# Kernel tuning notes

Hardware: AMD Instinct MI355X
Metric: run time of the kernel (lower is better)

The kernel has to match this reference:

```python
import jax, jax.numpy as jnp
import numpy as np

N_NODES = 50000


def _gcn_conv(h, W, b, src, dst, dinv):
    # PyG GCNConv: linear transform, then symmetric-normalized sum aggregation
    h = h @ W  # (N, d_out)
    norm = dinv[src] * dinv[dst]  # (E,)
    msg = h[src] * norm[:, None]  # (E, d_out)
    agg = jax.ops.segment_sum(msg, dst, num_segments=N_NODES)
    return agg + b


def setup_inputs() -> dict:
    key = jax.random.key(0)
    ks = jax.random.split(key, 9)
    in_dim, h1, h2, out_dim = 512, 512, 512, 256
    x = jax.random.normal(ks[0], (N_NODES, in_dim), dtype=jnp.float32)
    edge_index = jax.random.randint(ks[1], (2, 800000), 0, N_NODES, dtype=jnp.int64)

    def glorot(k, shape):
        lim = float(np.sqrt(6.0 / (shape[0] + shape[1])))
        return jax.random.uniform(k, shape, jnp.float32, -lim, lim)

    return {
        "x": x,
        "edge_index": edge_index,
        "W1": glorot(ks[2], (in_dim, h1)),
        "b1": jnp.zeros((h1,), jnp.float32),
        "W2": glorot(ks[3], (h1, h2)),
        "b2": jnp.zeros((h2,), jnp.float32),
        "Wout": glorot(ks[4], (h2, out_dim)),
        "bout": jnp.zeros((out_dim,), jnp.float32),
    }


def reference(x, edge_index, W1, b1, W2, b2, Wout, bout):
    # add self-loops (GCNConv default)
    loop = jnp.arange(N_NODES, dtype=edge_index.dtype)
    src = jnp.concatenate([edge_index[0], loop])
    dst = jnp.concatenate([edge_index[1], loop])
    # degree on A + I (target side), deg^{-1/2}
    deg = jax.ops.segment_sum(jnp.ones_like(dst, dtype=x.dtype), dst, num_segments=N_NODES)
    dinv = jnp.where(deg > 0, jax.lax.rsqrt(deg), 0.0)

    h = jax.nn.relu(_gcn_conv(x, W1, b1, src, dst, dinv))
    h = jax.nn.relu(_gcn_conv(h, W2, b2, src, dst, dinv))
    return h @ Wout + bout
```

## Files before the change

### kernel.cpp

```cpp
#include <hip/hip_runtime.h>

#define NN 50000
#define MP 50048
#define DD 512
#define EE 800000
#define NSCAN 196
#define SCB 3321
#define G1TILES 1564

typedef unsigned short u16;
typedef __attribute__((ext_vector_type(4))) float f32x4;
typedef __attribute__((ext_vector_type(8))) __bf16 bf16x8;
typedef __attribute__((ext_vector_type(8))) short s16x8;
typedef __attribute__((ext_vector_type(4))) short s16x4;

typedef __attribute__((address_space(1))) const void GVoid;
typedef __attribute__((address_space(3))) void LVoid;

__device__ __forceinline__ u16 f2bf(float f) {
  union { float f; unsigned u; } x; x.f = f;
  unsigned r = x.u + 0x7fffu + ((x.u >> 16) & 1u);
  return (u16)(r >> 16);
}
__device__ __forceinline__ float bf2f(u16 b) {
  union { unsigned u; float f; } x; x.u = ((unsigned)b) << 16;
  return x.f;
}


__global__ __launch_bounds__(256) void setup_k(int* __restrict__ cnt,
                                               const float* __restrict__ W1, u16* __restrict__ W1T,
                                               const float* __restrict__ W2, u16* __restrict__ W2T,
                                               const float* __restrict__ Wo, u16* __restrict__ WoT,
                                               int2* __restrict__ csr) {
  const int b = (int)blockIdx.x, t = threadIdx.x;
  if (b < 196) {
    int i = b * 256 + t;
    if (i < NN) cnt[i] = 1;
    if (b == 0 && t < 64) csr[EE + NN + t] = make_int2(0, 0);
    return;
  }
  const float* W; u16* WT; int ncols, idx;
  if (b < 1220)      { W = W1; WT = W1T; ncols = 512; idx = (b - 196) * 256 + t; }
  else if (b < 2244) { W = W2; WT = W2T; ncols = 512; idx = (b - 1220) * 256 + t; }
  else               { W = Wo; WT = WoT; ncols = 256; idx = (b - 2244) * 256 + t; }
  if (idx >= 512 * ncols) return;
  int n = idx >> 9, k = idx & 511;
  WT[idx] = f2bf(W[(size_t)k * ncols + n]);
}

__global__ __launch_bounds__(256) void count_k(const int* __restrict__ dst, int* __restrict__ cnt) {
  int e = blockIdx.x * 256 + threadIdx.x;
  if (e < EE) atomicAdd(&cnt[dst[e]], 1);
}


__global__ __launch_bounds__(256) void scan1_k(const int* __restrict__ cnt, int* __restrict__ bsum) {
  __shared__ int s[256];
  const int t = threadIdx.x;
  const int i = blockIdx.x * 256 + t;
  s[t] = (i < NN) ? cnt[i] : 0;
  __syncthreads();
  for (int off = 128; off > 0; off >>= 1) {
    if (t < off) s[t] += s[t + off];
    __syncthreads();
  }
  if (t == 0) bsum[blockIdx.x] = s[0];
}

__global__ __launch_bounds__(256) void scan2_k(const int* __restrict__ bsum, int* __restrict__ boff) {
  __shared__ int s[256];
  const int t = threadIdx.x;
  const int v = (t < NSCAN) ? bsum[t] : 0;
  s[t] = v;
  __syncthreads();
  for (int off = 1; off < 256; off <<= 1) {
    int a = s[t];
    int b = (t >= off) ? s[t - off] : 0;
    __syncthreads();
    s[t] = a + b;
    __syncthreads();
  }
  if (t < NSCAN) boff[t] = s[t] - v;
}

__global__ __launch_bounds__(256) void scan3_k(const int* __restrict__ cnt, const int* __restrict__ boff,
                                               int* __restrict__ rowp, int* __restrict__ cursor,
                                               float* __restrict__ dinv) {
  __shared__ int s[256];
  const int t = threadIdx.x;
  const int i = blockIdx.x * 256 + t;
  const int v = (i < NN) ? cnt[i] : 0;
  s[t] = v;
  __syncthreads();
  for (int off = 1; off < 256; off <<= 1) {
    int a = s[t];
    int b = (t >= off) ? s[t - off] : 0;
    __syncthreads();
    s[t] = a + b;
    __syncthreads();
  }
  const int excl = s[t] - v + boff[blockIdx.x];
  if (i < NN) {
    rowp[i] = excl; cursor[i] = excl;
    dinv[i] = rsqrtf((float)v);
  }
  if (i == NN - 1) rowp[NN] = excl + v;
}


__global__ __launch_bounds__(256) void gemm1_k(const float* __restrict__ X, const u16* __restrict__ BT,
                                               u16* __restrict__ C,
                                               const int* __restrict__ src, const int* __restrict__ dst,
                                               const float* __restrict__ dinv, int* __restrict__ cursor,
                                               int2* __restrict__ csr) {
  __shared__ u16 As[2][128 * 32];
  __shared__ u16 Bs[2][128 * 32];
  const int t = threadIdx.x;

  if (blockIdx.x < SCB) {
    int e = (int)blockIdx.x * 256 + t;
    if (e < EE) {
      int d = dst[e], sn = src[e];
      int pos = atomicAdd(&cursor[d], 1);
      csr[pos] = make_int2(sn, __float_as_int(dinv[sn] * dinv[d]));
    } else if (e < EE + NN) {
      int i = e - EE;
      int pos = atomicAdd(&cursor[i], 1);
      float di = dinv[i];
      csr[pos] = make_int2(i, __float_as_int(di * di));
    }
    return;
  }

  const int g = (int)blockIdx.x - SCB;
  const int xcd = g & 7;
  const int idx = g >> 3;
  const int q = G1TILES >> 3, r = G1TILES & 7;
  const int tile = (xcd < r ? xcd * (q + 1) : r * (q + 1) + (xcd - r) * q) + idx;
  const int bm = tile >> 2;
  const int bn = tile & 3;

  const int lane = t & 63;
  const int wc = (t >> 6) & 1;
  const int wr = (t >> 7) & 1;
  f32x4 acc[4][4] = {};
  const int r0 = t >> 2;
  const int kc = (t & 3) * 8;
  const int row1 = bm * 128 + 64 + r0;
  const float* Xp0 = X + (size_t)(bm * 128 + r0) * DD + kc;
  const float* Xp1 = X + (size_t)(row1 < NN ? row1 : NN - 1) * DD + kc;
  const u16* Bb = BT + (size_t)bn * 128 * DD + (size_t)r0 * DD + kc;

  f32x4 a0, a1, a2, a3;
  auto loadA = [&](int kt) {
    a0 = *(const f32x4*)(Xp0 + kt);
    a1 = *(const f32x4*)(Xp0 + kt + 4);
    a2 = *(const f32x4*)(Xp1 + kt);
    a3 = *(const f32x4*)(Xp1 + kt + 4);
  };
  auto writeA = [&](int buf) {
    bf16x8 w0, w1;
    #pragma unroll
    for (int j = 0; j < 4; ++j) {
      w0[j] = (__bf16)a0[j]; w0[4 + j] = (__bf16)a1[j];
      w1[j] = (__bf16)a2[j]; w1[4 + j] = (__bf16)a3[j];
    }
    *(bf16x8*)&As[buf][t * 8] = w0;
    *(bf16x8*)&As[buf][2048 + t * 8] = w1;
  };
  auto stageB = [&](int buf, int kt) {
    __builtin_amdgcn_global_load_lds((GVoid*)(Bb + kt),           (LVoid*)(&Bs[buf][t * 8]),        16, 0, 0);
    __builtin_amdgcn_global_load_lds((GVoid*)(Bb + 64 * DD + kt), (LVoid*)(&Bs[buf][2048 + t * 8]), 16, 0, 0);
  };

  loadA(0);
  stageB(0, 0);
  writeA(0);
  __syncthreads();

  #pragma unroll 2
  for (int step = 0; step < 16; ++step) {
    const int cur = step & 1;
    if (step < 15) { loadA((step + 1) * 32); stageB(cur ^ 1, (step + 1) * 32); }
    bf16x8 af[4], bv[4];
    #pragma unroll
    for (int m = 0; m < 4; ++m)
      af[m] = *(const bf16x8*)&As[cur][(wr * 64 + m * 16 + (lane & 15)) * 32 + (lane >> 4) * 8];
    #pragma unroll
    for (int n = 0; n < 4; ++n)
      bv[n] = *(const bf16x8*)&Bs[cur][(wc * 64 + n * 16 + (lane & 15)) * 32 + (lane >> 4) * 8];
    #pragma unroll
    for (int m = 0; m < 4; ++m) {
      #pragma unroll
      for (int n = 0; n < 4; ++n)
        acc[m][n] = __builtin_amdgcn_mfma_f32_16x16x32_bf16(af[m], bv[n], acc[m][n], 0, 0, 0);
    }
    if (step < 15) writeA(cur ^ 1);
    __syncthreads();
  }

  const int rb = bm * 128 + wr * 64 + ((lane >> 4) * 4);
  const int cb = bn * 128 + wc * 64 + (lane & 15);
  #pragma unroll
  for (int m = 0; m < 4; ++m) {
    #pragma unroll
    for (int rr = 0; rr < 4; ++rr) {
      const int row = rb + m * 16 + rr;
      if (row < NN) {
        #pragma unroll
        for (int n = 0; n < 4; ++n)
          C[(size_t)row * 512 + cb + n * 16] = f2bf(acc[m][n][rr]);
      }
    }
  }
}


template<int OUT_BF16>
__global__ __launch_bounds__(256) void gemm_k(const u16* __restrict__ A, const u16* __restrict__ BT,
                                              void* __restrict__ Cv, const float* __restrict__ bias,
                                              int M, int N) {
  const int nwg = (int)gridDim.x;
  const int id = (int)blockIdx.x;
  const int xcd = id & 7;
  const int idx = id >> 3;
  const int q = nwg >> 3, r = nwg & 7;
  const int tile = (xcd < r ? xcd * (q + 1) : r * (q + 1) + (xcd - r) * q) + idx;
  const int ntn = N >> 7;
  const int bm = tile / ntn;
  const int bn = tile % ntn;

  __shared__ u16 As[2][128 * 32];
  __shared__ u16 Bs[2][128 * 32];
  const int t = threadIdx.x;
  const int lane = t & 63;
  const int wc = (t >> 6) & 1;
  const int wr = (t >> 7) & 1;
  f32x4 acc[4][4] = {};
  const int r0 = t >> 2;
  const int kc = (t & 3) * 8;
  const u16* Ab = A + (size_t)bm * 128 * DD + (size_t)r0 * DD + kc;
  const u16* Bb = BT + (size_t)bn * 128 * DD + (size_t)r0 * DD + kc;

  auto stage = [&](int buf, int kt) {
    __builtin_amdgcn_global_load_lds((GVoid*)(Ab + kt),           (LVoid*)(&As[buf][t * 8]),        16, 0, 0);
    __builtin_amdgcn_global_load_lds((GVoid*)(Ab + 64 * DD + kt), (LVoid*)(&As[buf][2048 + t * 8]), 16, 0, 0);
    __builtin_amdgcn_global_load_lds((GVoid*)(Bb + kt),           (LVoid*)(&Bs[buf][t * 8]),        16, 0, 0);
    __builtin_amdgcn_global_load_lds((GVoid*)(Bb + 64 * DD + kt), (LVoid*)(&Bs[buf][2048 + t * 8]), 16, 0, 0);
  };

  stage(0, 0);
  __syncthreads();

  #pragma unroll 2
  for (int step = 0; step < 16; ++step) {
    const int cur = step & 1;
    if (step < 15) stage(cur ^ 1, (step + 1) * 32);
    bf16x8 af[4], bv[4];
    #pragma unroll
    for (int m = 0; m < 4; ++m)
      af[m] = *(const bf16x8*)&As[cur][(wr * 64 + m * 16 + (lane & 15)) * 32 + (lane >> 4) * 8];
    #pragma unroll
    for (int n = 0; n < 4; ++n)
      bv[n] = *(const bf16x8*)&Bs[cur][(wc * 64 + n * 16 + (lane & 15)) * 32 + (lane >> 4) * 8];
    #pragma unroll
    for (int m = 0; m < 4; ++m) {
      #pragma unroll
      for (int n = 0; n < 4; ++n)
        acc[m][n] = __builtin_amdgcn_mfma_f32_16x16x32_bf16(af[m], bv[n], acc[m][n], 0, 0, 0);
    }
    __syncthreads();
  }

  const int rb = bm * 128 + wr * 64 + ((lane >> 4) * 4);
  const int cb = bn * 128 + wc * 64 + (lane & 15);
  #pragma unroll
  for (int m = 0; m < 4; ++m) {
    #pragma unroll
    for (int rr = 0; rr < 4; ++rr) {
      const int row = rb + m * 16 + rr;
      if (row < M) {
        #pragma unroll
        for (int n = 0; n < 4; ++n) {
          const int col = cb + n * 16;
          float v = acc[m][n][rr];
          if (bias) v += bias[col];
          if (OUT_BF16) ((u16*)Cv)[(size_t)row * N + col] = f2bf(v);
          else          ((float*)Cv)[(size_t)row * N + col] = v;
        }
      }
    }
  }
}


__global__ __launch_bounds__(256) void aggregate_k(const u16* __restrict__ H, const int* __restrict__ rowp,
                                                   const int2* __restrict__ csr,
                                                   const float* __restrict__ bias,
                                                   u16* __restrict__ out) {
  const int slice = (int)blockIdx.x & 7;
  const int grp = (int)blockIdx.x >> 3;
  const int wid = threadIdx.x >> 6;
  const int lane = threadIdx.x & 63;
  const int g = lane >> 4;
  const int l = lane & 15;
  const int node = grp * 16 + wid * 4 + g;
  const int d0 = slice * 64 + l * 4;
  const int beg = rowp[node];
  const int dg = rowp[node + 1] - beg;
  const int rounds = (dg + 3) >> 2;
  const u16* Hd = H + d0;
  float a0 = 0.f, a1 = 0.f, a2 = 0.f, a3 = 0.f;

  int2 e0 = csr[beg], e1 = csr[beg + 1], e2 = csr[beg + 2], e3 = csr[beg + 3];
  for (int b = 0; b < rounds; ++b) {
    const int r = b * 4;
    const s16x4 v0 = *(const s16x4*)(Hd + (size_t)e0.x * DD);
    const s16x4 v1 = *(const s16x4*)(Hd + (size_t)e1.x * DD);
    const s16x4 v2 = *(const s16x4*)(Hd + (size_t)e2.x * DD);
    const s16x4 v3 = *(const s16x4*)(Hd + (size_t)e3.x * DD);
    const int nb = beg + r + 4;
    const int2 f0 = csr[nb], f1 = csr[nb + 1], f2 = csr[nb + 2], f3 = csr[nb + 3];
    const float w0 = (r + 0 < dg) ? __int_as_float(e0.y) : 0.f;
    const float w1 = (r + 1 < dg) ? __int_as_float(e1.y) : 0.f;
    const float w2 = (r + 2 < dg) ? __int_as_float(e2.y) : 0.f;
    const float w3 = (r + 3 < dg) ? __int_as_float(e3.y) : 0.f;
    a0 += bf2f((u16)v0[0]) * w0 + bf2f((u16)v1[0]) * w1 + bf2f((u16)v2[0]) * w2 + bf2f((u16)v3[0]) * w3;
    a1 += bf2f((u16)v0[1]) * w0 + bf2f((u16)v1[1]) * w1 + bf2f((u16)v2[1]) * w2 + bf2f((u16)v3[1]) * w3;
    a2 += bf2f((u16)v0[2]) * w0 + bf2f((u16)v1[2]) * w1 + bf2f((u16)v2[2]) * w2 + bf2f((u16)v3[2]) * w3;
    a3 += bf2f((u16)v0[3]) * w0 + bf2f((u16)v1[3]) * w1 + bf2f((u16)v2[3]) * w2 + bf2f((u16)v3[3]) * w3;
    e0 = f0; e1 = f1; e2 = f2; e3 = f3;
  }

  s16x4 o;
  o[0] = (short)f2bf(fmaxf(a0 + bias[d0 + 0], 0.f));
  o[1] = (short)f2bf(fmaxf(a1 + bias[d0 + 1], 0.f));
  o[2] = (short)f2bf(fmaxf(a2 + bias[d0 + 2], 0.f));
  o[3] = (short)f2bf(fmaxf(a3 + bias[d0 + 3], 0.f));
  *(s16x4*)(out + (size_t)node * DD + d0) = o;
}


extern "C" void kernel_launch(void* const* d_in, const int* in_sizes, int n_in,
                              void* d_out, int out_size, void* d_ws, size_t ws_size,
                              hipStream_t stream) {
  const float* x    = (const float*)d_in[0];
  const int*   ei   = (const int*)d_in[1];
  const float* W1   = (const float*)d_in[2];
  const float* b1   = (const float*)d_in[3];
  const float* W2   = (const float*)d_in[4];
  const float* b2   = (const float*)d_in[5];
  const float* Wout = (const float*)d_in[6];
  const float* bout = (const float*)d_in[7];
  float* out = (float*)d_out;
  (void)in_sizes; (void)n_in; (void)out_size; (void)ws_size;

  char* ws = (char*)d_ws;
  size_t off = 0;
  auto alloc = [&](size_t bytes) -> char* {
    char* p = ws + off;
    off = (off + bytes + 255) & ~(size_t)255;
    return p;
  };
  u16*   xb   = (u16*)alloc((size_t)MP * DD * 2);
  u16*   H    = (u16*)alloc((size_t)NN * DD * 2);
  u16*   W1T  = (u16*)alloc(512 * 512 * 2);
  u16*   W2T  = (u16*)alloc(512 * 512 * 2);
  u16*   WoT  = (u16*)alloc(256 * 512 * 2);
  int*   cnt  = (int*)alloc(NN * 4);
  float* dinv = (float*)alloc(NN * 4);
  int*   rowp = (int*)alloc((NN + 1) * 4);
  int*   cur  = (int*)alloc(NN * 4);
  int2*  csr  = (int2*)alloc((size_t)(EE + NN + 64) * 8);
  int*   bsum = (int*)alloc(NSCAN * 4);
  int*   boff = (int*)alloc(NSCAN * 4);

  const int* srcp = ei;
  const int* dstp = ei + EE;

  setup_k<<<2756, 256, 0, stream>>>(cnt, W1, W1T, W2, W2T, Wout, WoT, csr);
  count_k<<<(EE + 255) / 256, 256, 0, stream>>>(dstp, cnt);
  scan1_k<<<NSCAN, 256, 0, stream>>>(cnt, bsum);
  scan2_k<<<1, 256, 0, stream>>>(bsum, boff);
  scan3_k<<<NSCAN, 256, 0, stream>>>(cnt, boff, rowp, cur, dinv);

  const int agg_grid = (NN / 16) * 8;

  gemm1_k<<<SCB + G1TILES, 256, 0, stream>>>(x, W1T, H, srcp, dstp, dinv, cur, csr);
  aggregate_k<<<agg_grid, 256, 0, stream>>>(H, rowp, csr, b1, xb);
  gemm_k<1><<<(MP / 128) * (512 / 128), 256, 0, stream>>>(xb, W2T, (void*)H, nullptr, NN, 512);
  aggregate_k<<<agg_grid, 256, 0, stream>>>(H, rowp, csr, b2, xb);
  gemm_k<0><<<(MP / 128) * (256 / 128), 256, 0, stream>>>(xb, WoT, (void*)out, bout, NN, 256);
}
```

Measured before the change: 450.8 us.

## Pad CSR rows to multiples of four and pre-scale source indices to byte offsets

Each node's CSR segment is padded to a multiple of four entries, and the whole CSR buffer is zero-filled in the setup kernel. This lets the aggregation loop drop the per-edge bounds masks and read edge pairs as 128-bit int4 loads. Source indices are stored pre-shifted by 10, which is the byte offset of a 512-wide bf16 row, removing the index multiply in the gather. The cost is a larger CSR buffer and an extra zeroing pass, while zero-weight padded entries still issue row-0 loads.

```diff
diff --git a/kernel.cpp b/kernel.cpp
--- a/kernel.cpp
+++ b/kernel.cpp
@@ -7,6 +7,8 @@
 #define NSCAN 196
 #define SCB 3321
 #define G1TILES 1564
+#define CSRTOT (EE + NN + 3 * NN + 64)
+#define CSRZB 1954
 
 typedef unsigned short u16;
 typedef __attribute__((ext_vector_type(4))) float f32x4;
@@ -32,21 +34,21 @@
                                                const float* __restrict__ W1, u16* __restrict__ W1T,
                                                const float* __restrict__ W2, u16* __restrict__ W2T,
                                                const float* __restrict__ Wo, u16* __restrict__ WoT,
-                                               int2* __restrict__ csr) {
+                                               int4* __restrict__ csr4) {
   const int b = (int)blockIdx.x, t = threadIdx.x;
-  if (b < 196) {
-    int i = b * 256 + t;
-    if (i < NN) cnt[i] = 1;
-    if (b == 0 && t < 64) csr[EE + NN + t] = make_int2(0, 0);
+  if (b < 196) { int i = b * 256 + t; if (i < NN) cnt[i] = 1; return; }
+  if (b < 2756) {
+    const float* W; u16* WT; int ncols, idx;
+    if (b < 1220)      { W = W1; WT = W1T; ncols = 512; idx = (b - 196) * 256 + t; }
+    else if (b < 2244) { W = W2; WT = W2T; ncols = 512; idx = (b - 1220) * 256 + t; }
+    else               { W = Wo; WT = WoT; ncols = 256; idx = (b - 2244) * 256 + t; }
+    if (idx >= 512 * ncols) return;
+    int n = idx >> 9, k = idx & 511;
+    WT[idx] = f2bf(W[(size_t)k * ncols + n]);
     return;
   }
-  const float* W; u16* WT; int ncols, idx;
-  if (b < 1220)      { W = W1; WT = W1T; ncols = 512; idx = (b - 196) * 256 + t; }
-  else if (b < 2244) { W = W2; WT = W2T; ncols = 512; idx = (b - 1220) * 256 + t; }
-  else               { W = Wo; WT = WoT; ncols = 256; idx = (b - 2244) * 256 + t; }
-  if (idx >= 512 * ncols) return;
-  int n = idx >> 9, k = idx & 511;
-  WT[idx] = f2bf(W[(size_t)k * ncols + n]);
+  int idx = (b - 2756) * 256 + t;
+  if (idx < CSRTOT / 2) csr4[idx] = make_int4(0, 0, 0, 0);
 }
 
 __global__ __launch_bounds__(256) void count_k(const int* __restrict__ dst, int* __restrict__ cnt) {
@@ -59,7 +61,7 @@
   __shared__ int s[256];
   const int t = threadIdx.x;
   const int i = blockIdx.x * 256 + t;
-  s[t] = (i < NN) ? cnt[i] : 0;
+  s[t] = (i < NN) ? ((cnt[i] + 3) & ~3) : 0;
   __syncthreads();
   for (int off = 128; off > 0; off >>= 1) {
     if (t < off) s[t] += s[t + off];
@@ -91,7 +93,8 @@
   const int t = threadIdx.x;
   const int i = blockIdx.x * 256 + t;
   const int v = (i < NN) ? cnt[i] : 0;
-  s[t] = v;
+  const int pv = (v + 3) & ~3;
+  s[t] = pv;
   __syncthreads();
   for (int off = 1; off < 256; off <<= 1) {
     int a = s[t];
@@ -100,12 +103,12 @@
     s[t] = a + b;
     __syncthreads();
   }
-  const int excl = s[t] - v + boff[blockIdx.x];
+  const int excl = s[t] - pv + boff[blockIdx.x];
   if (i < NN) {
     rowp[i] = excl; cursor[i] = excl;
     dinv[i] = rsqrtf((float)v);
   }
-  if (i == NN - 1) rowp[NN] = excl + v;
+  if (i == NN - 1) rowp[NN] = excl + pv;
 }
 
 
@@ -123,12 +126,12 @@
     if (e < EE) {
       int d = dst[e], sn = src[e];
       int pos = atomicAdd(&cursor[d], 1);
-      csr[pos] = make_int2(sn, __float_as_int(dinv[sn] * dinv[d]));
+      csr[pos] = make_int2(sn << 10, __float_as_int(dinv[sn] * dinv[d]));
     } else if (e < EE + NN) {
       int i = e - EE;
       int pos = atomicAdd(&cursor[i], 1);
       float di = dinv[i];
-      csr[pos] = make_int2(i, __float_as_int(di * di));
+      csr[pos] = make_int2(i << 10, __float_as_int(di * di));
     }
     return;
   }
@@ -308,29 +311,25 @@
   const int node = grp * 16 + wid * 4 + g;
   const int d0 = slice * 64 + l * 4;
   const int beg = rowp[node];
-  const int dg = rowp[node + 1] - beg;
-  const int rounds = (dg + 3) >> 2;
-  const u16* Hd = H + d0;
+  const int rounds = (rowp[node + 1] - beg) >> 2;
+  const char* Hb = (const char*)H + (size_t)d0 * 2;
+  const int4* cp = (const int4*)(csr + beg);
   float a0 = 0.f, a1 = 0.f, a2 = 0.f, a3 = 0.f;
 
-  int2 e0 = csr[beg], e1 = csr[beg + 1], e2 = csr[beg + 2], e3 = csr[beg + 3];
+  int4 c01 = cp[0], c23 = cp[1];
   for (int b = 0; b < rounds; ++b) {
-    const int r = b * 4;
-    const s16x4 v0 = *(const s16x4*)(Hd + (size_t)e0.x * DD);
-    const s16x4 v1 = *(const s16x4*)(Hd + (size_t)e1.x * DD);
-    const s16x4 v2 = *(const s16x4*)(Hd + (size_t)e2.x * DD);
-    const s16x4 v3 = *(const s16x4*)(Hd + (size_t)e3.x * DD);
-    const int nb = beg + r + 4;
-    const int2 f0 = csr[nb], f1 = csr[nb + 1], f2 = csr[nb + 2], f3 = csr[nb + 3];
-    const float w0 = (r + 0 < dg) ? __int_as_float(e0.y) : 0.f;
-    const float w1 = (r + 1 < dg) ? __int_as_float(e1.y) : 0.f;
-    const float w2 = (r + 2 < dg) ? __int_as_float(e2.y) : 0.f;
-    const float w3 = (r + 3 < dg) ? __int_as_float(e3.y) : 0.f;
+    const s16x4 v0 = *(const s16x4*)(Hb + c01.x);
+    const s16x4 v1 = *(const s16x4*)(Hb + c01.z);
+    const s16x4 v2 = *(const s16x4*)(Hb + c23.x);
+    const s16x4 v3 = *(const s16x4*)(Hb + c23.z);
+    const int4 n01 = cp[2 * b + 2], n23 = cp[2 * b + 3];
+    const float w0 = __int_as_float(c01.y), w1 = __int_as_float(c01.w);
+    const float w2 = __int_as_float(c23.y), w3 = __int_as_float(c23.w);
     a0 += bf2f((u16)v0[0]) * w0 + bf2f((u16)v1[0]) * w1 + bf2f((u16)v2[0]) * w2 + bf2f((u16)v3[0]) * w3;
     a1 += bf2f((u16)v0[1]) * w0 + bf2f((u16)v1[1]) * w1 + bf2f((u16)v2[1]) * w2 + bf2f((u16)v3[1]) * w3;
     a2 += bf2f((u16)v0[2]) * w0 + bf2f((u16)v1[2]) * w1 + bf2f((u16)v2[2]) * w2 + bf2f((u16)v3[2]) * w3;
     a3 += bf2f((u16)v0[3]) * w0 + bf2f((u16)v1[3]) * w1 + bf2f((u16)v2[3]) * w2 + bf2f((u16)v3[3]) * w3;
-    e0 = f0; e1 = f1; e2 = f2; e3 = f3;
+    c01 = n01; c23 = n23;
   }
 
   s16x4 o;
@@ -372,14 +371,14 @@
   float* dinv = (float*)alloc(NN * 4);
   int*   rowp = (int*)alloc((NN + 1) * 4);
   int*   cur  = (int*)alloc(NN * 4);
-  int2*  csr  = (int2*)alloc((size_t)(EE + NN + 64) * 8);
+  int2*  csr  = (int2*)alloc((size_t)CSRTOT * 8);
   int*   bsum = (int*)alloc(NSCAN * 4);
   int*   boff = (int*)alloc(NSCAN * 4);
 
   const int* srcp = ei;
   const int* dstp = ei + EE;
 
-  setup_k<<<2756, 256, 0, stream>>>(cnt, W1, W1T, W2, W2T, Wout, WoT, csr);
+  setup_k<<<2756 + CSRZB, 256, 0, stream>>>(cnt, W1, W1T, W2, W2T, Wout, WoT, (int4*)csr);
   count_k<<<(EE + 255) / 256, 256, 0, stream>>>(dstp, cnt);
   scan1_k<<<NSCAN, 256, 0, stream>>>(cnt, bsum);
   scan2_k<<<1, 256, 0, stream>>>(bsum, boff);
```

Result: no change. 452.4 us (+0.4%).
